# Kernel optimization log

Measured on AMD Instinct MI355X. Metric: run time of the kernel, lower is better.

## Reference

```python
import jax, jax.numpy as jnp
import numpy as np

ITEM_NUM = 100000
H = 128          # hidden_size
L_PROTO = 500    # number of prototypes
K = 4            # top-k prototypes
SEQ = 50         # max_seq_length
B = 1024
TAO = 0.1
LAMBDA = 0.1
EPS = 1e-5


def layer_norm(x, g, b):
    mu = jnp.mean(x, axis=-1, keepdims=True)
    var = jnp.mean((x - mu) ** 2, axis=-1, keepdims=True)
    return (x - mu) * jax.lax.rsqrt(var + EPS) * g + b


def setup_inputs() -> dict:
    key = jax.random.key(0)
    ks = jax.random.split(key, 12)
    std = 0.02
    item_emb = jax.random.normal(ks[0], (ITEM_NUM, H), jnp.float32) * std
    item_emb = item_emb.at[0].set(0.0)  # padding_idx=0
    pos_emb = jax.random.normal(ks[1], (SEQ + 1, H), jnp.float32) * std
    pos_emb = pos_emb.at[0].set(0.0)    # padding_idx=0 (never hit when len==SEQ)
    proto = jax.random.normal(ks[2], (L_PROTO, H), jnp.float32) * std
    w1 = jax.random.normal(ks[3], (H, H), jnp.float32) * std
    w2 = jax.random.normal(ks[4], (H, 1), jnp.float32) * std
    w3 = jax.random.normal(ks[5], (H, H), jnp.float32) * std
    w4 = jax.random.normal(ks[6], (H, H), jnp.float32) * std
    w5 = jax.random.normal(ks[7], (H, K), jnp.float32) * std
    w6 = jax.random.normal(ks[8], (H, H), jnp.float32) * std
    w7 = jax.random.normal(ks[9], (H, 1), jnp.float32) * std
    seq = jax.random.randint(ks[10], (B, SEQ), 0, ITEM_NUM, dtype=jnp.int64)
    g = jnp.ones((H,), jnp.float32)
    b = jnp.zeros((H,), jnp.float32)
    return {
        'item_emb': item_emb, 'pos_emb': pos_emb, 'proto': proto,
        'w1': w1, 'w2': w2, 'w3': w3, 'w4': w4, 'w5': w5, 'w6': w6, 'w7': w7,
        'ln1_g': g, 'ln1_b': b, 'ln2_g': g, 'ln2_b': b,
        'ln3_g': g, 'ln3_b': b, 'ln4_g': g, 'ln4_b': b,
        'seq': seq,
    }


def reference(item_emb, pos_emb, proto, w1, w2, w3, w4, w5, w6, w7,
              ln1_g, ln1_b, ln2_g, ln2_b, ln3_g, ln3_b, ln4_g, ln4_b, seq):
    mask = (seq != 0).astype(jnp.float32)            # [B,S]
    ie = item_emb[seq]                               # [B,S,H]

    # self-attentive virtual concept vector
    sa_score = jnp.squeeze(jnp.tanh(ie @ w1) @ w2, -1)   # [B,S]
    sa_score = sa_score - (1.0 - mask) * 10000.0
    alpha = jax.nn.softmax(sa_score, axis=-1)
    vcv = jnp.einsum('bs,bsh->bh', alpha, ie)            # [B,H]

    # prototype routing: top-k by score
    s = vcv @ proto.T                                    # [B,L]
    chosen_s, rank = jax.lax.top_k(s, K)                 # [B,K]
    chosen_proto = proto[rank]                           # [B,K,H]
    chosen_proto = jax.nn.sigmoid(chosen_s)[..., None] * chosen_proto

    # item->prototype assignment
    p_kt_score = jnp.einsum('bsh,bkh->bsk',
                            layer_norm(ie @ w3, ln1_g, ln1_b),
                            layer_norm(chosen_proto, ln2_g, ln2_b))
    p_kt = jax.nn.softmax(p_kt_score, axis=-1) * mask[:, :, None]  # [B,S,K]

    # positional embedding (positions SEQ..1)
    position = SEQ - jnp.arange(SEQ)                     # [S]
    emb = pos_emb[position][None, :, :] + ie             # [B,S,H]

    a_k_score = jnp.swapaxes(jnp.tanh(emb @ w4) @ w5, 1, 2)   # [B,K,S]
    a_k = jax.nn.softmax(a_k_score, axis=-1) * mask[:, None, :]
    a_k = jnp.swapaxes(a_k, 1, 2)                        # [B,S,K]

    p = p_kt * a_k
    interesting = layer_norm(jnp.einsum('bsk,bsh->bkh', p, emb), ln3_g, ln3_b)  # [B,K,H]

    xu = jnp.einsum('bsk,bkh->bsh', p_kt, chosen_proto)  # [B,S,H]
    c_score = jnp.squeeze(jnp.tanh(xu @ w6) @ w7, -1) - (1.0 - mask) * 10000.0
    c_w = jax.nn.softmax(c_score, axis=-1)               # [B,S]
    c_apt = layer_norm(jnp.einsum('bs,bsh->bh', c_w, xu), ln4_g, ln4_b)  # [B,H]

    e_score = jnp.einsum('bh,bkh->bk', c_apt, interesting)
    e = jax.nn.softmax(e_score / TAO, axis=-1)
    final = jnp.einsum('bk,bkh->bh', e, interesting)     # [B,H]
    scores = final @ item_emb.T                          # [B,ITEM_NUM]

    # prototype covariance regularizer
    centered = proto - jnp.mean(proto, axis=0, keepdims=True)
    M = (centered @ centered.T) / H
    Lc = (jnp.linalg.norm(M) - jnp.linalg.norm(jnp.diag(M))) * 0.5
    return scores, LAMBDA * Lc
```

## Files before the change

### kernel.cpp

```cpp
#include <hip/hip_runtime.h>
#include <hip/hip_bf16.h>

#define H 128
#define H2 132
#define SQL 50
#define LPROTO 500
#define KTOP 4
#define BQ 1024
#define ITEMS 100000

typedef __attribute__((ext_vector_type(8))) short bf16x8;
typedef __attribute__((ext_vector_type(4))) float f32x4;

__device__ __forceinline__ float wsum(float v){
#pragma unroll
  for (int o = 32; o; o >>= 1) v += __shfl_xor(v, o, 64);
  return v;
}
__device__ __forceinline__ float wmax(float v){
#pragma unroll
  for (int o = 32; o; o >>= 1) v = fmaxf(v, __shfl_xor(v, o, 64));
  return v;
}
__device__ __forceinline__ unsigned short f2bf(float x){
  unsigned int u = __builtin_bit_cast(unsigned int, x);
  unsigned int r = u + 0x7fffu + ((u >> 16) & 1u);
  return (unsigned short)(r >> 16);
}
__device__ __forceinline__ float bf2f(unsigned short h){
  unsigned int u = ((unsigned int)h) << 16;
  return __builtin_bit_cast(float, u);
}

__device__ __forceinline__ void mm_mfma(const float (*src)[H2], float (*dst)[H2],
                                        const unsigned short* __restrict__ wt_hi,
                                        const unsigned short* __restrict__ wt_lo,
                                        int lane, int wave)
{
  const int r15 = lane & 15;
  const int g   = lane >> 4;
  const int kof = g * 8;
  const int row = wave * 16 + r15;
  const int srow = (row < SQL) ? row : 0;

  bf16x8 ah[4], al[4];
#pragma unroll
  for (int ks = 0; ks < 4; ks++){
    const float* p = &src[srow][ks * 32 + kof];
    float4 x0 = *reinterpret_cast<const float4*>(p);
    float4 x1 = *reinterpret_cast<const float4*>(p + 4);
    float xs[8] = {x0.x, x0.y, x0.z, x0.w, x1.x, x1.y, x1.z, x1.w};
    bf16x8 h, l;
#pragma unroll
    for (int e = 0; e < 8; e++){
      unsigned short hb = f2bf(xs[e]);
      float rem = xs[e] - bf2f(hb);
      h[e] = (short)hb;
      l[e] = (short)f2bf(rem);
    }
    ah[ks] = h; al[ks] = l;
  }

  f32x4 acc[8];
#pragma unroll
  for (int j = 0; j < 8; j++) acc[j] = (f32x4){0.f, 0.f, 0.f, 0.f};

#pragma unroll
  for (int j = 0; j < 8; j++){
    const unsigned short* bp = wt_hi + (j * 16 + r15) * H + kof;
    const unsigned short* lp = wt_lo + (j * 16 + r15) * H + kof;
    f32x4 a = acc[j];
#pragma unroll
    for (int ks = 0; ks < 4; ks++){
      bf16x8 bh = *reinterpret_cast<const bf16x8*>(bp + ks * 32);
      bf16x8 bl = *reinterpret_cast<const bf16x8*>(lp + ks * 32);
      a = __builtin_amdgcn_mfma_f32_16x16x32_bf16(ah[ks], bh, a, 0, 0, 0);
      a = __builtin_amdgcn_mfma_f32_16x16x32_bf16(al[ks], bh, a, 0, 0, 0);
      a = __builtin_amdgcn_mfma_f32_16x16x32_bf16(ah[ks], bl, a, 0, 0, 0);
    }
    acc[j] = a;
  }

#pragma unroll
  for (int j = 0; j < 8; j++){
#pragma unroll
    for (int r = 0; r < 4; r++){
      int orow = wave * 16 + g * 4 + r;
      if (orow < SQL) dst[orow][j * 16 + r15] = acc[j][r];
    }
  }
}

extern "C" __global__ __launch_bounds__(256)
void sine_row(const float* __restrict__ item_emb, const float* __restrict__ pos_emb,
              const float* __restrict__ proto,
              const float* __restrict__ w2, const float* __restrict__ w5,
              const float* __restrict__ w7,
              const unsigned short* __restrict__ wt,
              const float* __restrict__ ln1g, const float* __restrict__ ln1b,
              const float* __restrict__ ln2g, const float* __restrict__ ln2b,
              const float* __restrict__ ln3g, const float* __restrict__ ln3b,
              const float* __restrict__ ln4g, const float* __restrict__ ln4b,
              const int* __restrict__ seq,
              unsigned short* __restrict__ finalbf)
{
  __shared__ __align__(16) float sA[SQL][H2];
  __shared__ __align__(16) float sE[SQL][H2];
  __shared__ __align__(16) float scp[KTOP][H];
  __shared__ __align__(16) float slncp[KTOP][H];
  __shared__ __align__(16) float sintr[KTOP][H];
  __shared__ __align__(16) float svcv[H];
  __shared__ __align__(16) float scapt[H];
  __shared__ float srow[SQL];
  __shared__ float smask[SQL];
  __shared__ float spkt[SQL][KTOP];
  __shared__ float sak[SQL][KTOP];
  __shared__ float ssc[LPROTO];
  __shared__ float schs[KTOP];
  __shared__ int   srank[KTOP];
  __shared__ float sesc[KTOP];

  const int b = blockIdx.x;
  const int t = threadIdx.x;
  const int lane = t & 63;
  const int wave = t >> 6;
  const int* sq = seq + b * SQL;

  const unsigned short* w1t_hi = wt;
  const unsigned short* w1t_lo = wt + 16384;
  const unsigned short* w3t_hi = wt + 32768;
  const unsigned short* w3t_lo = wt + 49152;
  const unsigned short* w4t_hi = wt + 65536;
  const unsigned short* w4t_lo = wt + 81920;
  const unsigned short* w6t_hi = wt + 98304;
  const unsigned short* w6t_lo = wt + 114688;

  if (t < SQL) smask[t] = (sq[t] != 0) ? 1.0f : 0.0f;
  for (int c = t; c < SQL * (H / 4); c += 256){
    int s = c >> 5, q = c & 31;
    int idx = sq[s];
    float4 v = reinterpret_cast<const float4*>(item_emb)[idx * (H / 4) + q];
    reinterpret_cast<float4*>(&sA[s][0])[q] = v;
  }
  __syncthreads();

  mm_mfma(sA, sE, w1t_hi, w1t_lo, lane, wave);
  __syncthreads();
  for (int s = wave; s < SQL; s += 4){
    float y0 = sE[s][lane], y1 = sE[s][64 + lane];
    float part = tanhf(y0) * w2[lane] + tanhf(y1) * w2[64 + lane];
    float sc = wsum(part);
    if (lane == 0) srow[s] = sc - (1.0f - smask[s]) * 10000.0f;
  }
  __syncthreads();

  if (wave == 0){
    float v = (lane < SQL) ? srow[lane] : -1e30f;
    float m = wmax(v);
    float e = (lane < SQL) ? expf(v - m) : 0.0f;
    float sum = wsum(e);
    if (lane < SQL) srow[lane] = e / sum;
  }
  __syncthreads();
  if (t < H){
    float acc = 0.f;
    for (int s = 0; s < SQL; s++) acc = fmaf(srow[s], sA[s][t], acc);
    svcv[t] = acc;
  }
  __syncthreads();

  for (int l = t; l < LPROTO; l += 256){
    const float4* pr = reinterpret_cast<const float4*>(proto + l * H);
    const float4* vc = reinterpret_cast<const float4*>(svcv);
    float acc = 0.f;
    for (int q = 0; q < H / 4; q++){
      float4 p = pr[q], v = vc[q];
      acc += p.x * v.x + p.y * v.y + p.z * v.z + p.w * v.w;
    }
    ssc[l] = acc;
  }
  __syncthreads();
  if (wave == 0){
    float cand[8];
#pragma unroll
    for (int i = 0; i < 8; i++){
      int l = lane + 64 * i;
      cand[i] = (l < LPROTO) ? ssc[l] : -1e30f;
    }
    for (int k = 0; k < KTOP; k++){
      float bv = -1e30f; int bi = 0x7fffffff;
#pragma unroll
      for (int i = 0; i < 8; i++){
        int l = lane + 64 * i;
        if (cand[i] > bv || (cand[i] == bv && l < bi)){ bv = cand[i]; bi = l; }
      }
#pragma unroll
      for (int o = 32; o; o >>= 1){
        float ov = __shfl_xor(bv, o, 64);
        int   oi = __shfl_xor(bi, o, 64);
        if (ov > bv || (ov == bv && oi < bi)){ bv = ov; bi = oi; }
      }
      if (lane == 0){ schs[k] = bv; srank[k] = bi; }
      int li = bi - lane;
#pragma unroll
      for (int i = 0; i < 8; i++) if (64 * i == li) cand[i] = -1e30f;
    }
  }
  __syncthreads();
  {
    int k = wave;
    int r = srank[k];
    float sg = 1.0f / (1.0f + expf(-schs[k]));
    float v0 = sg * proto[r * H + lane];
    float v1 = sg * proto[r * H + 64 + lane];
    float mu = wsum(v0 + v1) * (1.0f / H);
    float d0 = v0 - mu, d1 = v1 - mu;
    float var = wsum(d0 * d0 + d1 * d1) * (1.0f / H);
    float rs = rsqrtf(var + 1e-5f);
    scp[k][lane] = v0; scp[k][64 + lane] = v1;
    slncp[k][lane]      = d0 * rs * ln2g[lane]      + ln2b[lane];
    slncp[k][64 + lane] = d1 * rs * ln2g[64 + lane] + ln2b[64 + lane];
  }
  __syncthreads();

  mm_mfma(sA, sE, w3t_hi, w3t_lo, lane, wave);
  __syncthreads();
  for (int s = wave; s < SQL; s += 4){
    float a0 = sE[s][lane], a1 = sE[s][64 + lane];
    float mu = wsum(a0 + a1) * (1.0f / H);
    float d0 = a0 - mu, d1 = a1 - mu;
    float var = wsum(d0 * d0 + d1 * d1) * (1.0f / H);
    float rs = rsqrtf(var + 1e-5f);
    float l0 = d0 * rs * ln1g[lane]      + ln1b[lane];
    float l1 = d1 * rs * ln1g[64 + lane] + ln1b[64 + lane];
    float sc0 = wsum(l0 * slncp[0][lane] + l1 * slncp[0][64 + lane]);
    float sc1 = wsum(l0 * slncp[1][lane] + l1 * slncp[1][64 + lane]);
    float sc2 = wsum(l0 * slncp[2][lane] + l1 * slncp[2][64 + lane]);
    float sc3 = wsum(l0 * slncp[3][lane] + l1 * slncp[3][64 + lane]);
    float m = fmaxf(fmaxf(sc0, sc1), fmaxf(sc2, sc3));
    float e0 = expf(sc0 - m), e1 = expf(sc1 - m), e2 = expf(sc2 - m), e3 = expf(sc3 - m);
    float inv = 1.0f / (e0 + e1 + e2 + e3);
    float msk = smask[s];
    if (lane == 0){
      spkt[s][0] = e0 * inv * msk; spkt[s][1] = e1 * inv * msk;
      spkt[s][2] = e2 * inv * msk; spkt[s][3] = e3 * inv * msk;
    }
  }
  __syncthreads();

  for (int c = t; c < SQL * (H / 4); c += 256){
    int s = c >> 5, q = c & 31;
    float4 pv = reinterpret_cast<const float4*>(pos_emb + (SQL - s) * H)[q];
    float4 iv = reinterpret_cast<float4*>(&sA[s][0])[q];
    float4 r; r.x = pv.x + iv.x; r.y = pv.y + iv.y; r.z = pv.z + iv.z; r.w = pv.w + iv.w;
    reinterpret_cast<float4*>(&sE[s][0])[q] = r;
  }
  __syncthreads();

  mm_mfma(sE, sA, w4t_hi, w4t_lo, lane, wave);
  __syncthreads();
  for (int s = wave; s < SQL; s += 4){
    float t0 = tanhf(sA[s][lane]), t1 = tanhf(sA[s][64 + lane]);
    float s0 = wsum(t0 * w5[lane * 4 + 0] + t1 * w5[(64 + lane) * 4 + 0]);
    float s1 = wsum(t0 * w5[lane * 4 + 1] + t1 * w5[(64 + lane) * 4 + 1]);
    float s2 = wsum(t0 * w5[lane * 4 + 2] + t1 * w5[(64 + lane) * 4 + 2]);
    float s3 = wsum(t0 * w5[lane * 4 + 3] + t1 * w5[(64 + lane) * 4 + 3]);
    if (lane == 0){ sak[s][0] = s0; sak[s][1] = s1; sak[s][2] = s2; sak[s][3] = s3; }
  }
  __syncthreads();

  {
    int k = wave;
    float v = (lane < SQL) ? sak[lane][k] : -1e30f;
    float m = wmax(v);
    float e = (lane < SQL) ? expf(v - m) : 0.0f;
    float sum = wsum(e);
    if (lane < SQL) sak[lane][k] = (e / sum) * smask[lane] * spkt[lane][k];
  }
  __syncthreads();

  for (int c = t; c < KTOP * H; c += 256){
    int k = c >> 7, h = c & 127;
    float acc = 0.f;
    for (int s = 0; s < SQL; s++) acc = fmaf(sak[s][k], sE[s][h], acc);
    sintr[k][h] = acc;
  }
  __syncthreads();
  {
    int k = wave;
    float v0 = sintr[k][lane], v1 = sintr[k][64 + lane];
    float mu = wsum(v0 + v1) * (1.0f / H);
    float d0 = v0 - mu, d1 = v1 - mu;
    float var = wsum(d0 * d0 + d1 * d1) * (1.0f / H);
    float rs = rsqrtf(var + 1e-5f);
    sintr[k][lane]      = d0 * rs * ln3g[lane]      + ln3b[lane];
    sintr[k][64 + lane] = d1 * rs * ln3g[64 + lane] + ln3b[64 + lane];
  }
  __syncthreads();

  for (int c = t; c < SQL * H; c += 256){
    int s = c >> 7, h = c & 127;
    float acc = spkt[s][0] * scp[0][h] + spkt[s][1] * scp[1][h]
              + spkt[s][2] * scp[2][h] + spkt[s][3] * scp[3][h];
    sA[s][h] = acc;
  }
  __syncthreads();
  mm_mfma(sA, sE, w6t_hi, w6t_lo, lane, wave);
  __syncthreads();
  for (int s = wave; s < SQL; s += 4){
    float part = tanhf(sE[s][lane]) * w7[lane] + tanhf(sE[s][64 + lane]) * w7[64 + lane];
    float sc = wsum(part);
    if (lane == 0) srow[s] = sc - (1.0f - smask[s]) * 10000.0f;
  }
  __syncthreads();

  if (wave == 0){
    float v = (lane < SQL) ? srow[lane] : -1e30f;
    float m = wmax(v);
    float e = (lane < SQL) ? expf(v - m) : 0.0f;
    float sum = wsum(e);
    if (lane < SQL) srow[lane] = e / sum;
  }
  __syncthreads();
  if (t < H){
    float acc = 0.f;
    for (int s = 0; s < SQL; s++) acc = fmaf(srow[s], sA[s][t], acc);
    scapt[t] = acc;
  }
  __syncthreads();
  if (wave == 0){
    float v0 = scapt[lane], v1 = scapt[64 + lane];
    float mu = wsum(v0 + v1) * (1.0f / H);
    float d0 = v0 - mu, d1 = v1 - mu;
    float var = wsum(d0 * d0 + d1 * d1) * (1.0f / H);
    float rs = rsqrtf(var + 1e-5f);
    scapt[lane]      = d0 * rs * ln4g[lane]      + ln4b[lane];
    scapt[64 + lane] = d1 * rs * ln4g[64 + lane] + ln4b[64 + lane];
  }
  __syncthreads();

  {
    int k = wave;
    float part = scapt[lane] * sintr[k][lane] + scapt[64 + lane] * sintr[k][64 + lane];
    float sc = wsum(part);
    if (lane == 0) sesc[k] = sc;
  }
  __syncthreads();
  if (t < H){
    float e0 = sesc[0] * 10.0f, e1 = sesc[1] * 10.0f, e2 = sesc[2] * 10.0f, e3 = sesc[3] * 10.0f;
    float m = fmaxf(fmaxf(e0, e1), fmaxf(e2, e3));
    float x0 = expf(e0 - m), x1 = expf(e1 - m), x2 = expf(e2 - m), x3 = expf(e3 - m);
    float inv = 1.0f / (x0 + x1 + x2 + x3);
    float f = (x0 * sintr[0][t] + x1 * sintr[1][t] + x2 * sintr[2][t] + x3 * sintr[3][t]) * inv;
    finalbf[b * H + t] = f2bf(f);
  }
}

extern "C" __global__ void wprep(const float* __restrict__ w1, const float* __restrict__ w3,
                                 const float* __restrict__ w4, const float* __restrict__ w6,
                                 unsigned short* __restrict__ out){
  const float* srcs[4] = {w1, w3, w4, w6};
  const float* src = srcs[blockIdx.x];
  unsigned short* hi = out + blockIdx.x * 32768;
  unsigned short* lo = hi + 16384;
  for (int i = threadIdx.x; i < 16384; i += 256){
    int c = i >> 7, k = i & 127;
    float f = src[k * H + c];
    unsigned short h = f2bf(f);
    hi[i] = h;
    lo[i] = f2bf(f - bf2f(h));
  }
}

extern "C" __global__ void conv_bf16(const float* __restrict__ in,
                                     unsigned short* __restrict__ out, int n4){
  int i = blockIdx.x * blockDim.x + threadIdx.x;
  int stride = gridDim.x * blockDim.x;
  for (; i < n4; i += stride){
    float4 v = reinterpret_cast<const float4*>(in)[i];
    union { unsigned short u[4]; uint2 v2; } o;
    o.u[0] = f2bf(v.x); o.u[1] = f2bf(v.y); o.u[2] = f2bf(v.z); o.u[3] = f2bf(v.w);
    reinterpret_cast<uint2*>(out)[i] = o.v2;
  }
}

#define GBM 64
#define GBN 128
#define LDT 136

extern "C" __global__ __launch_bounds__(256)
void gemm_scores(const unsigned short* __restrict__ A,
                 const unsigned short* __restrict__ Bm,
                 float* __restrict__ C)
{
  __shared__ __align__(16) unsigned short sA[GBM][LDT];
  __shared__ __align__(16) unsigned short sB[GBN][LDT];
  const int t = threadIdx.x, lane = t & 63, wave = t >> 6;
  const int n0 = blockIdx.x * GBN;
  const int m0 = blockIdx.y * GBM;

  for (int c = t; c < GBM * 16; c += 256){
    int r = c >> 4, q = c & 15;
    uint4 v = reinterpret_cast<const uint4*>(A + (m0 + r) * H)[q];
    *reinterpret_cast<uint4*>(&sA[r][q * 8]) = v;
  }
  for (int c = t; c < GBN * 16; c += 256){
    int r = c >> 4, q = c & 15;
    int n = n0 + r;
    uint4 v = make_uint4(0u, 0u, 0u, 0u);
    if (n < ITEMS) v = reinterpret_cast<const uint4*>(Bm + n * H)[q];
    *reinterpret_cast<uint4*>(&sB[r][q * 8]) = v;
  }
  __syncthreads();

  const int wm = wave >> 1, wn = wave & 1;
  f32x4 acc[2][4];
#pragma unroll
  for (int i = 0; i < 2; i++)
#pragma unroll
    for (int j = 0; j < 4; j++) acc[i][j] = (f32x4){0.f, 0.f, 0.f, 0.f};

#pragma unroll
  for (int ks = 0; ks < 4; ks++){
    bf16x8 af[2], bfr[4];
#pragma unroll
    for (int i = 0; i < 2; i++)
      af[i] = *reinterpret_cast<const bf16x8*>(&sA[wm * 32 + i * 16 + (lane & 15)][ks * 32 + (lane >> 4) * 8]);
#pragma unroll
    for (int j = 0; j < 4; j++)
      bfr[j] = *reinterpret_cast<const bf16x8*>(&sB[wn * 64 + j * 16 + (lane & 15)][ks * 32 + (lane >> 4) * 8]);
#pragma unroll
    for (int i = 0; i < 2; i++)
#pragma unroll
      for (int j = 0; j < 4; j++)
        acc[i][j] = __builtin_amdgcn_mfma_f32_16x16x32_bf16(af[i], bfr[j], acc[i][j], 0, 0, 0);
  }

#pragma unroll
  for (int i = 0; i < 2; i++){
    int mrow = m0 + wm * 32 + i * 16 + (lane >> 4) * 4;
#pragma unroll
    for (int j = 0; j < 4; j++){
      int ncol = n0 + wn * 64 + j * 16 + (lane & 15);
      if (ncol < ITEMS){
#pragma unroll
        for (int r = 0; r < 4; r++)
          C[(size_t)(mrow + r) * ITEMS + ncol] = acc[i][j][r];
      }
    }
  }
}

extern "C" __global__ void proto_mean(const float* __restrict__ proto,
                                      float* __restrict__ mean, float* __restrict__ accum){
  int h = threadIdx.x;
  if (h < 2) accum[h] = 0.0f;
  float acc = 0.f;
  for (int l = 0; l < LPROTO; l++) acc += proto[l * H + h];
  mean[h] = acc * (1.0f / LPROTO);
}

extern "C" __global__ __launch_bounds__(256)
void proto_cov(const float* __restrict__ proto, const float* __restrict__ mean,
               float* __restrict__ accum){
  __shared__ float ci[H];
  __shared__ float red[256];
  int i = blockIdx.x, t = threadIdx.x;
  if (t < H) ci[t] = proto[i * H + t] - mean[t];
  __syncthreads();
  float total = 0.f;
  for (int j = t; j < LPROTO; j += 256){
    float acc = 0.f;
    for (int h = 0; h < H; h++) acc = fmaf(ci[h], proto[j * H + h] - mean[h], acc);
    float m = acc * (1.0f / H);
    total += m * m;
    if (j == i) atomicAdd(&accum[1], m * m);
  }
  red[t] = total; __syncthreads();
  for (int o = 128; o; o >>= 1){ if (t < o) red[t] += red[t + o]; __syncthreads(); }
  if (t == 0) atomicAdd(&accum[0], red[0]);
}

extern "C" __global__ void lc_final(const float* __restrict__ accum, float* __restrict__ out){
  out[(size_t)BQ * ITEMS] = 0.1f * 0.5f * (sqrtf(accum[0]) - sqrtf(accum[1]));
}

extern "C" void kernel_launch(void* const* d_in, const int* in_sizes, int n_in,
                              void* d_out, int out_size, void* d_ws, size_t ws_size,
                              hipStream_t stream){
  const float* item  = (const float*)d_in[0];
  const float* pos   = (const float*)d_in[1];
  const float* proto = (const float*)d_in[2];
  const float* w1 = (const float*)d_in[3];
  const float* w2 = (const float*)d_in[4];
  const float* w3 = (const float*)d_in[5];
  const float* w4 = (const float*)d_in[6];
  const float* w5 = (const float*)d_in[7];
  const float* w6 = (const float*)d_in[8];
  const float* w7 = (const float*)d_in[9];
  const float* ln1g = (const float*)d_in[10];
  const float* ln1b = (const float*)d_in[11];
  const float* ln2g = (const float*)d_in[12];
  const float* ln2b = (const float*)d_in[13];
  const float* ln3g = (const float*)d_in[14];
  const float* ln3b = (const float*)d_in[15];
  const float* ln4g = (const float*)d_in[16];
  const float* ln4b = (const float*)d_in[17];
  const int* seq = (const int*)d_in[18];
  float* out = (float*)d_out;

  char* ws = (char*)d_ws;
  float* accum = (float*)ws;
  float* mean  = (float*)(ws + 256);
  unsigned short* finalbf = (unsigned short*)(ws + 1024);
  unsigned short* itembf  = (unsigned short*)(ws + 263168);
  unsigned short* wtbuf   = (unsigned short*)(ws + 25863168);

  wprep<<<4, 256, 0, stream>>>(w1, w3, w4, w6, wtbuf);
  conv_bf16<<<2048, 256, 0, stream>>>(item, itembf, ITEMS * H / 4);

  sine_row<<<BQ, 256, 0, stream>>>(item, pos, proto, w2, w5, w7, wtbuf,
                                   ln1g, ln1b, ln2g, ln2b, ln3g, ln3b, ln4g, ln4b,
                                   seq, finalbf);

  gemm_scores<<<dim3((ITEMS + GBN - 1) / GBN, BQ / GBM), 256, 0, stream>>>(finalbf, itembf, out);

  proto_mean<<<1, 128, 0, stream>>>(proto, mean, accum);
  proto_cov<<<LPROTO, 256, 0, stream>>>(proto, mean, accum);
  lc_final<<<1, 1, 0, stream>>>(accum, out);
}
```

Measured before the change: 429.7 us.

## Widen sine_row to 512 threads and rewrite scores GEMM with transposed operands

```diff
diff --git a/kernel.cpp b/kernel.cpp
--- a/kernel.cpp
+++ b/kernel.cpp
@@ -40,7 +40,9 @@
   const int r15 = lane & 15;
   const int g   = lane >> 4;
   const int kof = g * 8;
-  const int row = wave * 16 + r15;
+  const int tile = wave >> 1;
+  const int jbase = (wave & 1) * 4;
+  const int row = tile * 16 + r15;
   const int srow = (row < SQL) ? row : 0;
 
   bf16x8 ah[4], al[4];
@@ -61,15 +63,16 @@
     ah[ks] = h; al[ks] = l;
   }
 
-  f32x4 acc[8];
-#pragma unroll
-  for (int j = 0; j < 8; j++) acc[j] = (f32x4){0.f, 0.f, 0.f, 0.f};
-
-#pragma unroll
-  for (int j = 0; j < 8; j++){
+  f32x4 acc[4];
+#pragma unroll
+  for (int jj = 0; jj < 4; jj++) acc[jj] = (f32x4){0.f, 0.f, 0.f, 0.f};
+
+#pragma unroll
+  for (int jj = 0; jj < 4; jj++){
+    int j = jbase + jj;
     const unsigned short* bp = wt_hi + (j * 16 + r15) * H + kof;
     const unsigned short* lp = wt_lo + (j * 16 + r15) * H + kof;
-    f32x4 a = acc[j];
+    f32x4 a = acc[jj];
 #pragma unroll
     for (int ks = 0; ks < 4; ks++){
       bf16x8 bh = *reinterpret_cast<const bf16x8*>(bp + ks * 32);
@@ -78,20 +81,21 @@
       a = __builtin_amdgcn_mfma_f32_16x16x32_bf16(al[ks], bh, a, 0, 0, 0);
       a = __builtin_amdgcn_mfma_f32_16x16x32_bf16(ah[ks], bl, a, 0, 0, 0);
     }
-    acc[j] = a;
-  }
-
-#pragma unroll
-  for (int j = 0; j < 8; j++){
+    acc[jj] = a;
+  }
+
+#pragma unroll
+  for (int jj = 0; jj < 4; jj++){
+    int j = jbase + jj;
 #pragma unroll
     for (int r = 0; r < 4; r++){
-      int orow = wave * 16 + g * 4 + r;
-      if (orow < SQL) dst[orow][j * 16 + r15] = acc[j][r];
-    }
-  }
-}
-
-extern "C" __global__ __launch_bounds__(256)
+      int orow = tile * 16 + g * 4 + r;
+      if (orow < SQL) dst[orow][j * 16 + r15] = acc[jj][r];
+    }
+  }
+}
+
+extern "C" __global__ __launch_bounds__(512)
 void sine_row(const float* __restrict__ item_emb, const float* __restrict__ pos_emb,
               const float* __restrict__ proto,
               const float* __restrict__ w2, const float* __restrict__ w5,
@@ -136,7 +140,7 @@
   const unsigned short* w6t_lo = wt + 114688;
 
   if (t < SQL) smask[t] = (sq[t] != 0) ? 1.0f : 0.0f;
-  for (int c = t; c < SQL * (H / 4); c += 256){
+  for (int c = t; c < SQL * (H / 4); c += 512){
     int s = c >> 5, q = c & 31;
     int idx = sq[s];
     float4 v = reinterpret_cast<const float4*>(item_emb)[idx * (H / 4) + q];
@@ -146,7 +150,7 @@
 
   mm_mfma(sA, sE, w1t_hi, w1t_lo, lane, wave);
   __syncthreads();
-  for (int s = wave; s < SQL; s += 4){
+  for (int s = wave; s < SQL; s += 8){
     float y0 = sE[s][lane], y1 = sE[s][64 + lane];
     float part = tanhf(y0) * w2[lane] + tanhf(y1) * w2[64 + lane];
     float sc = wsum(part);
@@ -169,7 +173,7 @@
   }
   __syncthreads();
 
-  for (int l = t; l < LPROTO; l += 256){
+  for (int l = t; l < LPROTO; l += 512){
     const float4* pr = reinterpret_cast<const float4*>(proto + l * H);
     const float4* vc = reinterpret_cast<const float4*>(svcv);
     float acc = 0.f;
@@ -207,7 +211,7 @@
     }
   }
   __syncthreads();
-  {
+  if (wave < KTOP){
     int k = wave;
     int r = srank[k];
     float sg = 1.0f / (1.0f + expf(-schs[k]));
@@ -225,7 +229,7 @@
 
   mm_mfma(sA, sE, w3t_hi, w3t_lo, lane, wave);
   __syncthreads();
-  for (int s = wave; s < SQL; s += 4){
+  for (int s = wave; s < SQL; s += 8){
     float a0 = sE[s][lane], a1 = sE[s][64 + lane];
     float mu = wsum(a0 + a1) * (1.0f / H);
     float d0 = a0 - mu, d1 = a1 - mu;
@@ -248,7 +252,7 @@
   }
   __syncthreads();
 
-  for (int c = t; c < SQL * (H / 4); c += 256){
+  for (int c = t; c < SQL * (H / 4); c += 512){
     int s = c >> 5, q = c & 31;
     float4 pv = reinterpret_cast<const float4*>(pos_emb + (SQL - s) * H)[q];
     float4 iv = reinterpret_cast<float4*>(&sA[s][0])[q];
@@ -259,7 +263,7 @@
 
   mm_mfma(sE, sA, w4t_hi, w4t_lo, lane, wave);
   __syncthreads();
-  for (int s = wave; s < SQL; s += 4){
+  for (int s = wave; s < SQL; s += 8){
     float t0 = tanhf(sA[s][lane]), t1 = tanhf(sA[s][64 + lane]);
     float s0 = wsum(t0 * w5[lane * 4 + 0] + t1 * w5[(64 + lane) * 4 + 0]);
     float s1 = wsum(t0 * w5[lane * 4 + 1] + t1 * w5[(64 + lane) * 4 + 1]);
@@ -269,7 +273,7 @@
   }
   __syncthreads();
 
-  {
+  if (wave < KTOP){
     int k = wave;
     float v = (lane < SQL) ? sak[lane][k] : -1e30f;
     float m = wmax(v);
@@ -279,14 +283,14 @@
   }
   __syncthreads();
 
-  for (int c = t; c < KTOP * H; c += 256){
+  for (int c = t; c < KTOP * H; c += 512){
     int k = c >> 7, h = c & 127;
     float acc = 0.f;
     for (int s = 0; s < SQL; s++) acc = fmaf(sak[s][k], sE[s][h], acc);
     sintr[k][h] = acc;
   }
   __syncthreads();
-  {
+  if (wave < KTOP){
     int k = wave;
     float v0 = sintr[k][lane], v1 = sintr[k][64 + lane];
     float mu = wsum(v0 + v1) * (1.0f / H);
@@ -298,7 +302,7 @@
   }
   __syncthreads();
 
-  for (int c = t; c < SQL * H; c += 256){
+  for (int c = t; c < SQL * H; c += 512){
     int s = c >> 7, h = c & 127;
     float acc = spkt[s][0] * scp[0][h] + spkt[s][1] * scp[1][h]
               + spkt[s][2] * scp[2][h] + spkt[s][3] * scp[3][h];
@@ -307,7 +311,7 @@
   __syncthreads();
   mm_mfma(sA, sE, w6t_hi, w6t_lo, lane, wave);
   __syncthreads();
-  for (int s = wave; s < SQL; s += 4){
+  for (int s = wave; s < SQL; s += 8){
     float part = tanhf(sE[s][lane]) * w7[lane] + tanhf(sE[s][64 + lane]) * w7[64 + lane];
     float sc = wsum(part);
     if (lane == 0) srow[s] = sc - (1.0f - smask[s]) * 10000.0f;
@@ -339,7 +343,7 @@
   }
   __syncthreads();
 
-  {
+  if (wave < KTOP){
     int k = wave;
     float part = scapt[lane] * sintr[k][lane] + scapt[64 + lane] * sintr[k][64 + lane];
     float sc = wsum(part);
@@ -384,69 +388,45 @@
   }
 }
 
-#define GBM 64
-#define GBN 128
-#define LDT 136
-
 extern "C" __global__ __launch_bounds__(256)
-void gemm_scores(const unsigned short* __restrict__ A,
-                 const unsigned short* __restrict__ Bm,
+void gemm_scores(const unsigned short* __restrict__ Bm,
+                 const unsigned short* __restrict__ A,
                  float* __restrict__ C)
 {
-  __shared__ __align__(16) unsigned short sA[GBM][LDT];
-  __shared__ __align__(16) unsigned short sB[GBN][LDT];
-  const int t = threadIdx.x, lane = t & 63, wave = t >> 6;
-  const int n0 = blockIdx.x * GBN;
-  const int m0 = blockIdx.y * GBM;
-
-  for (int c = t; c < GBM * 16; c += 256){
-    int r = c >> 4, q = c & 15;
-    uint4 v = reinterpret_cast<const uint4*>(A + (m0 + r) * H)[q];
-    *reinterpret_cast<uint4*>(&sA[r][q * 8]) = v;
-  }
-  for (int c = t; c < GBN * 16; c += 256){
-    int r = c >> 4, q = c & 15;
-    int n = n0 + r;
-    uint4 v = make_uint4(0u, 0u, 0u, 0u);
-    if (n < ITEMS) v = reinterpret_cast<const uint4*>(Bm + n * H)[q];
-    *reinterpret_cast<uint4*>(&sB[r][q * 8]) = v;
-  }
-  __syncthreads();
-
-  const int wm = wave >> 1, wn = wave & 1;
-  f32x4 acc[2][4];
-#pragma unroll
-  for (int i = 0; i < 2; i++)
-#pragma unroll
-    for (int j = 0; j < 4; j++) acc[i][j] = (f32x4){0.f, 0.f, 0.f, 0.f};
-
-#pragma unroll
-  for (int ks = 0; ks < 4; ks++){
-    bf16x8 af[2], bfr[4];
-#pragma unroll
-    for (int i = 0; i < 2; i++)
-      af[i] = *reinterpret_cast<const bf16x8*>(&sA[wm * 32 + i * 16 + (lane & 15)][ks * 32 + (lane >> 4) * 8]);
-#pragma unroll
-    for (int j = 0; j < 4; j++)
-      bfr[j] = *reinterpret_cast<const bf16x8*>(&sB[wn * 64 + j * 16 + (lane & 15)][ks * 32 + (lane >> 4) * 8]);
-#pragma unroll
-    for (int i = 0; i < 2; i++)
-#pragma unroll
-      for (int j = 0; j < 4; j++)
-        acc[i][j] = __builtin_amdgcn_mfma_f32_16x16x32_bf16(af[i], bfr[j], acc[i][j], 0, 0, 0);
-  }
-
-#pragma unroll
-  for (int i = 0; i < 2; i++){
-    int mrow = m0 + wm * 32 + i * 16 + (lane >> 4) * 4;
-#pragma unroll
-    for (int j = 0; j < 4; j++){
-      int ncol = n0 + wn * 64 + j * 16 + (lane & 15);
-      if (ncol < ITEMS){
-#pragma unroll
-        for (int r = 0; r < 4; r++)
-          C[(size_t)(mrow + r) * ITEMS + ncol] = acc[i][j][r];
-      }
+  const int lane = threadIdx.x & 63, wave = threadIdx.x >> 6;
+  const int r15 = lane & 15, g = lane >> 4;
+  const int nb = blockIdx.x * 64 + wave * 16;
+  const int m0 = blockIdx.y * 256;
+
+  const int irow = nb + r15;
+  const int it = (irow < ITEMS) ? irow : 0;
+  bf16x8 af[4];
+#pragma unroll
+  for (int ks = 0; ks < 4; ks++)
+    af[ks] = *reinterpret_cast<const bf16x8*>(Bm + (size_t)it * H + ks * 32 + g * 8);
+
+  f32x4 acc[16];
+#pragma unroll
+  for (int j = 0; j < 16; j++) acc[j] = (f32x4){0.f, 0.f, 0.f, 0.f};
+
+#pragma unroll
+  for (int j = 0; j < 16; j++){
+    const unsigned short* fp = A + (m0 + j * 16 + r15) * H + g * 8;
+    f32x4 a = acc[j];
+#pragma unroll
+    for (int ks = 0; ks < 4; ks++){
+      bf16x8 bf = *reinterpret_cast<const bf16x8*>(fp + ks * 32);
+      a = __builtin_amdgcn_mfma_f32_16x16x32_bf16(af[ks], bf, a, 0, 0, 0);
+    }
+    acc[j] = a;
+  }
+
+  const int n = nb + g * 4;
+  if (n < ITEMS){
+#pragma unroll
+    for (int j = 0; j < 16; j++){
+      int m = m0 + j * 16 + r15;
+      *reinterpret_cast<f32x4*>(C + (size_t)m * ITEMS + n) = acc[j];
     }
   }
 }
@@ -519,11 +499,11 @@
   wprep<<<4, 256, 0, stream>>>(w1, w3, w4, w6, wtbuf);
   conv_bf16<<<2048, 256, 0, stream>>>(item, itembf, ITEMS * H / 4);
 
-  sine_row<<<BQ, 256, 0, stream>>>(item, pos, proto, w2, w5, w7, wtbuf,
+  sine_row<<<BQ, 512, 0, stream>>>(item, pos, proto, w2, w5, w7, wtbuf,
                                    ln1g, ln1b, ln2g, ln2b, ln3g, ln3b, ln4g, ln4b,
                                    seq, finalbf);
 
-  gemm_scores<<<dim3((ITEMS + GBN - 1) / GBN, BQ / GBM), 256, 0, stream>>>(finalbf, itembf, out);
+  gemm_scores<<<dim3((ITEMS + 63) / 64, BQ / 256), 256, 0, stream>>>(itembf, finalbf, out);
 
   proto_mean<<<1, 128, 0, stream>>>(proto, mean, accum);
   proto_cov<<<LPROTO, 256, 0, stream>>>(proto, mean, accum);
```

After: 590.7 us. +37.5%, slower.
